# Optimization experiments

Hardware: AMD Instinct MI355X
Metric: run time of the kernel (lower is better)

Reference implementation:

```python
import jax, jax.numpy as jnp
import numpy as np

DIM = 512
HIDDEN = 1024
NUM_EXPERTS = 8
TOP_K = 2
BALANCE_LOSS_WEIGHT = 0.01


def setup_inputs() -> dict:
    key = jax.random.key(0)
    ks = jax.random.split(key, 6)
    B, S = 4, 8192
    x = jax.random.normal(ks[0], (B, S, DIM), dtype=jnp.float32)
    # Linear params (stored already transposed for x @ W convenience)
    scale_in = 1.0 / np.sqrt(DIM)
    scale_hid = 1.0 / np.sqrt(HIDDEN)
    gate_w = jax.random.uniform(ks[1], (DIM, NUM_EXPERTS), jnp.float32, -scale_in, scale_in)
    w1 = jax.random.uniform(ks[2], (NUM_EXPERTS, DIM, HIDDEN), jnp.float32, -scale_in, scale_in)
    b1 = jax.random.uniform(ks[3], (NUM_EXPERTS, HIDDEN), jnp.float32, -scale_in, scale_in)
    w2 = jax.random.uniform(ks[4], (NUM_EXPERTS, HIDDEN, DIM), jnp.float32, -scale_hid, scale_hid)
    b2 = jax.random.uniform(ks[5], (NUM_EXPERTS, DIM), jnp.float32, -scale_hid, scale_hid)
    return {"x": x, "gate_w": gate_w, "w1": w1, "b1": b1, "w2": w2, "b2": b2}


def reference(x, gate_w, w1, b1, w2, b2):
    B, S, D = x.shape
    T = B * S
    E = gate_w.shape[1]
    flat_x = x.reshape(T, D)

    # Gating (eval mode: no noise)
    gate_logits = flat_x @ gate_w                      # [T, E]
    gates = jax.nn.softmax(gate_logits, axis=-1)
    top_k_gates, top_k_indices = jax.lax.top_k(gates, TOP_K)
    top_k_gates = top_k_gates / jnp.sum(top_k_gates, axis=-1, keepdims=True)

    rows = jnp.arange(T)[:, None]
    # Per-token combine weight for each expert (0 if not selected)
    combine_w = jnp.zeros((T, E), flat_x.dtype).at[rows, top_k_indices].add(top_k_gates)
    # Load-balance loss (indices are discrete -> constant mask)
    expert_mask = jnp.zeros((T, E), flat_x.dtype).at[rows, top_k_indices].set(1.0)
    expert_usage = expert_mask.sum(0) / T
    balance_loss = jnp.mean((expert_usage - 1.0 / E) ** 2) * E * BALANCE_LOSS_WEIGHT

    # Expert MLPs; unselected tokens have combine weight 0 so contribute nothing,
    # matching the original masked gather/scatter math exactly.
    out = jnp.zeros_like(flat_x)
    for e in range(E):  # small fixed expert count
        h = jax.nn.gelu(flat_x @ w1[e] + b1[e], approximate=False)  # [T, HIDDEN]
        out = out + (h @ w2[e] + b2[e]) * combine_w[:, e:e + 1]
    return out.reshape(B, S, D), balance_loss
```

## Files before the change

### kernel.cpp

```cpp
#include <hip/hip_runtime.h>
#include <stdint.h>

#define T_TOK 32768
#define DDIM 512
#define HID 1024
#define NEXP 8

typedef _Float16 f16;
typedef _Float16 f16x8 __attribute__((ext_vector_type(8)));
typedef _Float16 f16x4 __attribute__((ext_vector_type(4)));
typedef float f32x4 __attribute__((ext_vector_type(4)));

__device__ __forceinline__ void gload_lds16(const void* g, void* l) {
  __builtin_amdgcn_global_load_lds(
      (__attribute__((address_space(1))) void*)g,
      (__attribute__((address_space(3))) void*)l, 16, 0, 0);
}

__global__ void k_cvt_x(const float* __restrict__ x, f16* __restrict__ xh) {
  int i = blockIdx.x * blockDim.x + threadIdx.x;
  float4 v = ((const float4*)x)[i];
  f16x4 o = {(f16)v.x, (f16)v.y, (f16)v.z, (f16)v.w};
  ((f16x4*)xh)[i] = o;
}

__global__ void k_transpose(const float* __restrict__ W, f16* __restrict__ Wt,
                            const int K, const int N) {
  __shared__ float tile[64][65];
  const int e = blockIdx.z;
  const float* Wb = W + (size_t)e * K * N;
  f16* Wtb = Wt + (size_t)e * K * N;
  const int k0 = blockIdx.x * 64, n0 = blockIdx.y * 64;
  const int tr = threadIdx.x >> 2;
  const int tc = (threadIdx.x & 3) * 16;
#pragma unroll
  for (int j = 0; j < 16; j += 4) {
    float4 v = *(const float4*)&Wb[(size_t)(k0 + tr) * N + n0 + tc + j];
    tile[tr][tc + j + 0] = v.x; tile[tr][tc + j + 1] = v.y;
    tile[tr][tc + j + 2] = v.z; tile[tr][tc + j + 3] = v.w;
  }
  __syncthreads();
  f16x8 t0, t1;
#pragma unroll
  for (int j = 0; j < 8; ++j) {
    t0[j] = (f16)tile[tc + j][tr];
    t1[j] = (f16)tile[tc + 8 + j][tr];
  }
  *(f16x8*)&Wtb[(size_t)(n0 + tr) * K + k0 + tc] = t0;
  *(f16x8*)&Wtb[(size_t)(n0 + tr) * K + k0 + tc + 8] = t1;
}

__global__ void k_gate(const float* __restrict__ x, const float* __restrict__ gw,
                       int* __restrict__ route_e, float* __restrict__ route_w,
                       int* __restrict__ cnt) {
  __shared__ int scnt[NEXP];
  const int tid = threadIdx.x, lane = tid & 63, wv = tid >> 6;
  if (tid < NEXP) scnt[tid] = 0;
  __syncthreads();

  float ga[4][8], gb[4][8];
#pragma unroll
  for (int j = 0; j < 4; ++j) {
    const int r0 = lane * 4 + j;
    const int r1 = 256 + lane * 4 + j;
    float4 q0 = *(const float4*)&gw[r0 * 8];
    float4 q1 = *(const float4*)&gw[r0 * 8 + 4];
    ga[j][0] = q0.x; ga[j][1] = q0.y; ga[j][2] = q0.z; ga[j][3] = q0.w;
    ga[j][4] = q1.x; ga[j][5] = q1.y; ga[j][6] = q1.z; ga[j][7] = q1.w;
    q0 = *(const float4*)&gw[r1 * 8];
    q1 = *(const float4*)&gw[r1 * 8 + 4];
    gb[j][0] = q0.x; gb[j][1] = q0.y; gb[j][2] = q0.z; gb[j][3] = q0.w;
    gb[j][4] = q1.x; gb[j][5] = q1.y; gb[j][6] = q1.z; gb[j][7] = q1.w;
  }

  const int tbase = blockIdx.x * 32 + wv * 8;
  for (int it = 0; it < 8; ++it) {
    const int t = tbase + it;
    const float4 A = *(const float4*)&x[(size_t)t * DDIM + lane * 4];
    const float4 B = *(const float4*)&x[(size_t)t * DDIM + 256 + lane * 4];
    float p[8];
#pragma unroll
    for (int e = 0; e < 8; ++e) {
      p[e] = A.x * ga[0][e] + A.y * ga[1][e] + A.z * ga[2][e] + A.w * ga[3][e] +
             B.x * gb[0][e] + B.y * gb[1][e] + B.z * gb[2][e] + B.w * gb[3][e];
    }
#pragma unroll
    for (int off = 32; off >= 1; off >>= 1) {
#pragma unroll
      for (int e = 0; e < 8; ++e) p[e] += __shfl_xor(p[e], off);
    }
    if (lane == 0) {
      int e1 = 0;
#pragma unroll
      for (int e = 1; e < 8; ++e) if (p[e] > p[e1]) e1 = e;
      int e2 = (e1 == 0) ? 1 : 0;
#pragma unroll
      for (int e = 0; e < 8; ++e) if (e != e1 && p[e] > p[e2]) e2 = e;
      const float wa = 1.0f / (1.0f + expf(p[e2] - p[e1]));
      route_e[t] = e1 | (e2 << 8);
      route_w[t] = wa;
      atomicAdd(&scnt[e1], 1);
      atomicAdd(&scnt[e2], 1);
    }
  }
  __syncthreads();
  if (tid < NEXP) atomicAdd(&cnt[tid], scnt[tid]);
}

__global__ void k_scan(const int* __restrict__ cnt, int* __restrict__ base,
                       int* __restrict__ cursor, float* __restrict__ out_loss) {
  if (threadIdx.x == 0) {
    int b = 0;
    float loss = 0.0f;
    for (int e = 0; e < NEXP; ++e) {
      base[e] = b;
      cursor[e] = b;
      b += cnt[e];
      float u = (float)cnt[e] / (float)T_TOK - 0.125f;
      loss += u * u;
    }
    *out_loss = loss * 0.01f;
  }
}

__global__ void k_scatter(const int* __restrict__ route_e, const float* __restrict__ route_w,
                          int* __restrict__ cursor, int* __restrict__ tok_slot,
                          float* __restrict__ wgt_slot) {
  const int t = blockIdx.x * blockDim.x + threadIdx.x;
  const int lane = threadIdx.x & 63;
  const int re = route_e[t];
  const float wa = route_w[t];
  const int e1 = re & 0xff, e2 = re >> 8;
#pragma unroll
  for (int e = 0; e < NEXP; ++e) {
    unsigned long long m = __ballot(e1 == e);
    if (m) {
      const int leader = __ffsll(m) - 1;
      int b0 = 0;
      if (lane == leader) b0 = atomicAdd(&cursor[e], __popcll(m));
      b0 = __shfl(b0, leader);
      if (e1 == e) {
        const int pos = b0 + __popcll(m & ((1ull << lane) - 1));
        tok_slot[pos] = t;
        wgt_slot[pos] = wa;
      }
    }
    m = __ballot(e2 == e);
    if (m) {
      const int leader = __ffsll(m) - 1;
      int b0 = 0;
      if (lane == leader) b0 = atomicAdd(&cursor[e], __popcll(m));
      b0 = __shfl(b0, leader);
      if (e2 == e) {
        const int pos = b0 + __popcll(m & ((1ull << lane) - 1));
        tok_slot[pos] = t;
        wgt_slot[pos] = 1.0f - wa;
      }
    }
  }
}


#define STAGE_G(k0_)                                                \
  do {                                                              \
    _Pragma("unroll") for (int i = 0; i < 4; ++i) {                 \
      gload_lds16(aSrc[i] + (k0_), &As0[(wv * 4 + i) * 512]);       \
      gload_lds16(bSrc[i] + (k0_), &Bs0[(wv * 4 + i) * 512]);       \
    }                                                               \
  } while (0)

#define COMPUTE(As_, Bs_)                                                         \
  do {                                                                            \
    _Pragma("unroll") for (int kb = 0; kb < 2; ++kb) {                            \
      f16x8 af[4], bf[4];                                                         \
      _Pragma("unroll") for (int mf = 0; mf < 4; ++mf) {                          \
        const int row = wm * 64 + mf * 16 + l15;                                  \
        af[mf] = *(const f16x8*)&(As_)[row * 64 + (((kb * 4 + g) ^ (row & 7)) * 8)]; \
      }                                                                           \
      _Pragma("unroll") for (int nf = 0; nf < 4; ++nf) {                          \
        const int row = wn * 64 + nf * 16 + l15;                                  \
        bf[nf] = *(const f16x8*)&(Bs_)[row * 64 + (((kb * 4 + g) ^ (row & 7)) * 8)]; \
      }                                                                           \
      _Pragma("unroll") for (int mf = 0; mf < 4; ++mf)                            \
        _Pragma("unroll") for (int nf = 0; nf < 4; ++nf)                          \
          acc[mf][nf] =                                                           \
              __builtin_amdgcn_mfma_f32_16x16x32_f16(af[mf], bf[nf], acc[mf][nf], 0, 0, 0); \
    }                                                                             \
  } while (0)

#define PIPE_LOOP(NT_)                                              \
  do {                                                              \
    for (int t = 0; t < (NT_); ++t) {                               \
      STAGE_G(t * 64);                                              \
      __syncthreads();             \
      COMPUTE(As0, Bs0);                                            \
      __syncthreads();                       \
    }                                                               \
  } while (0)

#define DECODE_SWZ(nN_)                                             \
  const int grp = 8 * (nN_);                                        \
  const int m_lin = (blockIdx.x / grp) * 8 + (blockIdx.x & 7);      \
  const int n0t = (blockIdx.x % grp) >> 3;                          \
  const int e = m_lin >> 6;                                         \
  const int mt = m_lin & 63;

__global__ __launch_bounds__(256, 4) void k_mlp1(
    const f16* __restrict__ xh, const f16* __restrict__ w1t,
    const float* __restrict__ b1, f16* __restrict__ h,
    const int* __restrict__ tok_slot, const int* __restrict__ base,
    const int* __restrict__ cnt, const int hc, const int c0, const int nN) {
  DECODE_SWZ(nN);
  const int ne = cnt[e];
  const int n0 = n0t * 128;
  const int sbase = base[e];
  const int shi = sbase + ne;

  __shared__ f16 As0[128 * 64];
  __shared__ f16 Bs0[128 * 64];

  const int tid = threadIdx.x;
  const int lane = tid & 63;
  const int wv = tid >> 6;
  const int wm = wv >> 1, wn = wv & 1;
  const int g = lane >> 4;
  const int l15 = lane & 15;

  for (int m0 = mt * 128; m0 < ne; m0 += 8192) {
    const int slot0 = sbase + m0;

    const f16* aSrc[4];
    const f16* bSrc[4];
#pragma unroll
    for (int i = 0; i < 4; ++i) {
      const int ch = wv * 4 + i;
      const int row = ch * 8 + (lane >> 3);
      const int sw = ((lane & 7) ^ (row & 7)) * 8;
      int slot = slot0 + row;
      slot = (slot <= shi - 1) ? slot : (shi - 1);
      const int tok = tok_slot[slot];
      aSrc[i] = xh + (size_t)tok * DDIM + sw;
      bSrc[i] = w1t + (size_t)(e * HID + c0 + n0 + row) * DDIM + sw;
    }

    f32x4 acc[4][4];
#pragma unroll
    for (int a = 0; a < 4; ++a)
#pragma unroll
      for (int b = 0; b < 4; ++b) { f32x4 z = {0.f, 0.f, 0.f, 0.f}; acc[a][b] = z; }

    PIPE_LOOP(DDIM / 64);

#pragma unroll
    for (int mf = 0; mf < 4; ++mf) {
#pragma unroll
      for (int r = 0; r < 4; ++r) {
        const int row = wm * 64 + mf * 16 + g * 4 + r;
        const int oslot = slot0 + row;
        if (oslot >= shi) continue;
#pragma unroll
        for (int nf = 0; nf < 4; ++nf) {
          const int col = wn * 64 + nf * 16 + l15;
          float v = acc[mf][nf][r] + b1[e * HID + c0 + n0 + col];
          v = 0.5f * v * (1.0f + erff(v * 0.70710678118654752f));
          h[(size_t)oslot * hc + n0 + col] = (f16)v;
        }
      }
    }
  }
}

__global__ __launch_bounds__(256, 4) void k_mlp2(
    const f16* __restrict__ h, const f16* __restrict__ w2t,
    const float* __restrict__ b2, float* __restrict__ out,
    const int* __restrict__ tok_slot, const float* __restrict__ wgt_slot,
    const int* __restrict__ base, const int* __restrict__ cnt,
    const int hc, const int c0) {
  DECODE_SWZ(4);
  const int ne = cnt[e];
  const int n0 = n0t * 128;
  const int sbase = base[e];
  const int shi = sbase + ne;

  __shared__ f16 As0[128 * 64];
  __shared__ f16 Bs0[128 * 64];

  const int tid = threadIdx.x;
  const int lane = tid & 63;
  const int wv = tid >> 6;
  const int wm = wv >> 1, wn = wv & 1;
  const int g = lane >> 4;
  const int l15 = lane & 15;

  for (int m0 = mt * 128; m0 < ne; m0 += 8192) {
    const int slot0 = sbase + m0;

    const f16* aSrc[4];
    const f16* bSrc[4];
#pragma unroll
    for (int i = 0; i < 4; ++i) {
      const int ch = wv * 4 + i;
      const int row = ch * 8 + (lane >> 3);
      const int sw = ((lane & 7) ^ (row & 7)) * 8;
      int slot = slot0 + row;
      slot = (slot <= shi - 1) ? slot : (shi - 1);
      aSrc[i] = h + (size_t)slot * hc + sw;
      bSrc[i] = w2t + (size_t)(e * DDIM + n0 + row) * HID + c0 + sw;
    }

    f32x4 acc[4][4];
#pragma unroll
    for (int a = 0; a < 4; ++a)
#pragma unroll
      for (int b = 0; b < 4; ++b) { f32x4 z = {0.f, 0.f, 0.f, 0.f}; acc[a][b] = z; }

    PIPE_LOOP(hc / 64);

#pragma unroll
    for (int mf = 0; mf < 4; ++mf) {
#pragma unroll
      for (int r = 0; r < 4; ++r) {
        const int row = wm * 64 + mf * 16 + g * 4 + r;
        const int oslot = slot0 + row;
        if (oslot >= shi) continue;
        const int tok = tok_slot[oslot];
        const float w = wgt_slot[oslot];
        float* orow = out + (size_t)tok * DDIM + n0;
#pragma unroll
        for (int nf = 0; nf < 4; ++nf) {
          const int col = wn * 64 + nf * 16 + l15;
          float v = acc[mf][nf][r];
          if (c0 == 0) v += b2[e * DDIM + n0 + col];
          unsafeAtomicAdd(orow + col, w * v);
        }
      }
    }
  }
}

extern "C" void kernel_launch(void* const* d_in, const int* in_sizes, int n_in,
                              void* d_out, int out_size, void* d_ws, size_t ws_size,
                              hipStream_t stream) {
  (void)in_sizes; (void)n_in;
  const float* x  = (const float*)d_in[0];
  const float* gw = (const float*)d_in[1];
  const float* w1 = (const float*)d_in[2];
  const float* b1 = (const float*)d_in[3];
  const float* w2 = (const float*)d_in[4];
  const float* b2 = (const float*)d_in[5];
  float* out = (float*)d_out;

  char* ws = (char*)d_ws;
  size_t off = 0;
  auto alloc = [&](size_t bytes) {
    char* p = ws + off;
    off += (bytes + 255) & ~(size_t)255;
    return p;
  };
  f16*   xh       = (f16*)  alloc((size_t)T_TOK * DDIM * 2);
  f16*   w1t      = (f16*)  alloc((size_t)NEXP * DDIM * HID * 2);
  f16*   w2t      = (f16*)  alloc((size_t)NEXP * DDIM * HID * 2);
  int*   route_e  = (int*)  alloc((size_t)T_TOK * 4);
  float* route_w  = (float*)alloc((size_t)T_TOK * 4);
  int*   tok_slot = (int*)  alloc((size_t)2 * T_TOK * 4);
  float* wgt_slot = (float*)alloc((size_t)2 * T_TOK * 4);
  int*   cnt      = (int*)  alloc(256);
  int*   base     = cnt + 8;
  int*   cursor   = cnt + 16;
  f16*   hbuf     = (f16*)(ws + off);
  const size_t havail = (ws_size > off) ? (ws_size - off) : 0;

  int ns = 4;
  const int cands[3] = {1, 2, 4};
  for (int i = 0; i < 3; ++i) {
    if ((size_t)2 * T_TOK * (HID / cands[i]) * 2 <= havail) { ns = cands[i]; break; }
  }
  const int hc = HID / ns;

  hipMemsetAsync(cnt, 0, 32, stream);
  hipMemsetAsync(d_out, 0, (size_t)out_size * sizeof(float), stream);

  k_cvt_x<<<dim3(T_TOK * DDIM / 4 / 256), 256, 0, stream>>>(x, xh);
  k_transpose<<<dim3(DDIM / 64, HID / 64, NEXP), 256, 0, stream>>>(w1, w1t, DDIM, HID);
  k_transpose<<<dim3(HID / 64, DDIM / 64, NEXP), 256, 0, stream>>>(w2, w2t, HID, DDIM);
  k_gate<<<dim3(T_TOK / 32), 256, 0, stream>>>(x, gw, route_e, route_w, cnt);
  k_scan<<<1, 64, 0, stream>>>(cnt, base, cursor, out + (size_t)T_TOK * DDIM);
  k_scatter<<<dim3(T_TOK / 256), 256, 0, stream>>>(route_e, route_w, cursor, tok_slot, wgt_slot);

  for (int c = 0; c < ns; ++c) {
    const int nN1 = hc / 128;
    k_mlp1<<<dim3(512 * nN1), 256, 0, stream>>>(
        xh, w1t, b1, hbuf, tok_slot, base, cnt, hc, c * hc, nN1);
    k_mlp2<<<dim3(512 * 4), 256, 0, stream>>>(
        hbuf, w2t, b2, out, tok_slot, wgt_slot, base, cnt, hc, c * hc);
  }
}
```

Baseline: 655.9 us.

## Widen MoE GEMM tiles to 128x256 with 512-thread blocks and unified LDS

Both expert GEMM kernels move from 128x128 output tiles with 4 waves to 128x256 tiles with 8 waves, staging A and B through one 384-row shared buffer. Each block now loads its gathered activation tile once for twice as many output columns, which cuts repeated A-side gathers and global traffic per flop. Block indexing changes from a swizzled grouping to expert-interleaved ordering, and a barrier is added at the end of each m-loop iteration. In exchange there are half as many blocks, more LDS per block, and lower occupancy.

```diff
diff --git a/kernel.cpp b/kernel.cpp
--- a/kernel.cpp
+++ b/kernel.cpp
@@ -163,23 +163,22 @@
 
 #define STAGE_G(k0_)                                                \
   do {                                                              \
-    _Pragma("unroll") for (int i = 0; i < 4; ++i) {                 \
-      gload_lds16(aSrc[i] + (k0_), &As0[(wv * 4 + i) * 512]);       \
-      gload_lds16(bSrc[i] + (k0_), &Bs0[(wv * 4 + i) * 512]);       \
+    _Pragma("unroll") for (int i = 0; i < 6; ++i) {                 \
+      gload_lds16(srcP[i] + (k0_), &S[(wv * 6 + i) * 512]);         \
     }                                                               \
   } while (0)
 
-#define COMPUTE(As_, Bs_)                                                         \
+#define COMPUTE()                                                                 \
   do {                                                                            \
     _Pragma("unroll") for (int kb = 0; kb < 2; ++kb) {                            \
       f16x8 af[4], bf[4];                                                         \
       _Pragma("unroll") for (int mf = 0; mf < 4; ++mf) {                          \
         const int row = wm * 64 + mf * 16 + l15;                                  \
-        af[mf] = *(const f16x8*)&(As_)[row * 64 + (((kb * 4 + g) ^ (row & 7)) * 8)]; \
+        af[mf] = *(const f16x8*)&S[row * 64 + (((kb * 4 + g) ^ (row & 7)) * 8)];  \
       }                                                                           \
       _Pragma("unroll") for (int nf = 0; nf < 4; ++nf) {                          \
-        const int row = wn * 64 + nf * 16 + l15;                                  \
-        bf[nf] = *(const f16x8*)&(Bs_)[row * 64 + (((kb * 4 + g) ^ (row & 7)) * 8)]; \
+        const int row = 128 + wn * 64 + nf * 16 + l15;                            \
+        bf[nf] = *(const f16x8*)&S[row * 64 + (((kb * 4 + g) ^ (row & 7)) * 8)];  \
       }                                                                           \
       _Pragma("unroll") for (int mf = 0; mf < 4; ++mf)                            \
         _Pragma("unroll") for (int nf = 0; nf < 4; ++nf)                          \
@@ -192,55 +191,56 @@
   do {                                                              \
     for (int t = 0; t < (NT_); ++t) {                               \
       STAGE_G(t * 64);                                              \
-      __syncthreads();             \
-      COMPUTE(As0, Bs0);                                            \
-      __syncthreads();                       \
+      __syncthreads();                                              \
+      COMPUTE();                                                    \
+      __syncthreads();                                              \
     }                                                               \
   } while (0)
 
-#define DECODE_SWZ(nN_)                                             \
-  const int grp = 8 * (nN_);                                        \
-  const int m_lin = (blockIdx.x / grp) * 8 + (blockIdx.x & 7);      \
-  const int n0t = (blockIdx.x % grp) >> 3;                          \
-  const int e = m_lin >> 6;                                         \
-  const int mt = m_lin & 63;
-
-__global__ __launch_bounds__(256, 4) void k_mlp1(
+__global__ __launch_bounds__(512, 2) void k_mlp1(
     const f16* __restrict__ xh, const f16* __restrict__ w1t,
     const float* __restrict__ b1, f16* __restrict__ h,
     const int* __restrict__ tok_slot, const int* __restrict__ base,
     const int* __restrict__ cnt, const int hc, const int c0, const int nN) {
-  DECODE_SWZ(nN);
+  const int e = blockIdx.x & 7;
+  const int q = blockIdx.x >> 3;
+  const int nt = q % nN;
+  const int mt = q / nN;
   const int ne = cnt[e];
-  const int n0 = n0t * 128;
+  const int n0 = nt * 256;
   const int sbase = base[e];
   const int shi = sbase + ne;
 
-  __shared__ f16 As0[128 * 64];
-  __shared__ f16 Bs0[128 * 64];
+  __shared__ f16 S[384 * 64];
 
   const int tid = threadIdx.x;
   const int lane = tid & 63;
   const int wv = tid >> 6;
-  const int wm = wv >> 1, wn = wv & 1;
+  const int wm = wv >> 2, wn = wv & 3;
   const int g = lane >> 4;
   const int l15 = lane & 15;
 
-  for (int m0 = mt * 128; m0 < ne; m0 += 8192) {
+  int sRow[6], sSw[6];
+#pragma unroll
+  for (int i = 0; i < 6; ++i) {
+    const int s = (wv * 6 + i) * 64 + lane;
+    sRow[i] = s >> 3;
+    sSw[i] = ((s & 7) ^ (sRow[i] & 7)) * 8;
+  }
+
+  for (int m0 = mt * 128; m0 < ne; m0 += 64 * 128) {
     const int slot0 = sbase + m0;
 
-    const f16* aSrc[4];
-    const f16* bSrc[4];
-#pragma unroll
-    for (int i = 0; i < 4; ++i) {
-      const int ch = wv * 4 + i;
-      const int row = ch * 8 + (lane >> 3);
-      const int sw = ((lane & 7) ^ (row & 7)) * 8;
-      int slot = slot0 + row;
-      slot = (slot <= shi - 1) ? slot : (shi - 1);
-      const int tok = tok_slot[slot];
-      aSrc[i] = xh + (size_t)tok * DDIM + sw;
-      bSrc[i] = w1t + (size_t)(e * HID + c0 + n0 + row) * DDIM + sw;
+    const f16* srcP[6];
+#pragma unroll
+    for (int i = 0; i < 6; ++i) {
+      if (sRow[i] < 128) {
+        int slot = slot0 + sRow[i];
+        slot = (slot <= shi - 1) ? slot : (shi - 1);
+        srcP[i] = xh + (size_t)tok_slot[slot] * DDIM + sSw[i];
+      } else {
+        srcP[i] = w1t + (size_t)(e * HID + c0 + n0 + sRow[i] - 128) * DDIM + sSw[i];
+      }
     }
 
     f32x4 acc[4][4];
@@ -267,45 +267,55 @@
         }
       }
     }
-  }
-}
-
-__global__ __launch_bounds__(256, 4) void k_mlp2(
+    __syncthreads();
+  }
+}
+
+__global__ __launch_bounds__(512, 2) void k_mlp2(
     const f16* __restrict__ h, const f16* __restrict__ w2t,
     const float* __restrict__ b2, float* __restrict__ out,
     const int* __restrict__ tok_slot, const float* __restrict__ wgt_slot,
     const int* __restrict__ base, const int* __restrict__ cnt,
     const int hc, const int c0) {
-  DECODE_SWZ(4);
+  const int e = blockIdx.x & 7;
+  const int q = blockIdx.x >> 3;
+  const int nt = q & 1;
+  const int mt = q >> 1;
   const int ne = cnt[e];
-  const int n0 = n0t * 128;
+  const int n0 = nt * 256;
   const int sbase = base[e];
   const int shi = sbase + ne;
 
-  __shared__ f16 As0[128 * 64];
-  __shared__ f16 Bs0[128 * 64];
+  __shared__ f16 S[384 * 64];
 
   const int tid = threadIdx.x;
   const int lane = tid & 63;
   const int wv = tid >> 6;
-  const int wm = wv >> 1, wn = wv & 1;
+  const int wm = wv >> 2, wn = wv & 3;
   const int g = lane >> 4;
   const int l15 = lane & 15;
 
-  for (int m0 = mt * 128; m0 < ne; m0 += 8192) {
+  int sRow[6], sSw[6];
+#pragma unroll
+  for (int i = 0; i < 6; ++i) {
+    const int s = (wv * 6 + i) * 64 + lane;
+    sRow[i] = s >> 3;
+    sSw[i] = ((s & 7) ^ (sRow[i] & 7)) * 8;
+  }
+
+  for (int m0 = mt * 128; m0 < ne; m0 += 64 * 128) {
     const int slot0 = sbase + m0;
 
-    const f16* aSrc[4];
-    const f16* bSrc[4];
-#pragma unroll
-    for (int i = 0; i < 4; ++i) {
-      const int ch = wv * 4 + i;
-      const int row = ch * 8 + (lane >> 3);
-      const int sw = ((lane & 7) ^ (row & 7)) * 8;
-      int slot = slot0 + row;
-      slot = (slot <= shi - 1) ? slot : (shi - 1);
-      aSrc[i] = h + (size_t)slot * hc + sw;
-      bSrc[i] = w2t + (size_t)(e * DDIM + n0 + row) * HID + c0 + sw;
+    const f16* srcP[6];
+#pragma unroll
+    for (int i = 0; i < 6; ++i) {
+      if (sRow[i] < 128) {
+        int slot = slot0 + sRow[i];
+        slot = (slot <= shi - 1) ? slot : (shi - 1);
+        srcP[i] = h + (size_t)slot * hc + sSw[i];
+      } else {
+        srcP[i] = w2t + (size_t)(e * DDIM + n0 + sRow[i] - 128) * HID + c0 + sSw[i];
+      }
     }
 
     f32x4 acc[4][4];
@@ -335,6 +345,7 @@
         }
       }
     }
+    __syncthreads();
   }
 }
 
@@ -388,10 +399,10 @@
   k_scatter<<<dim3(T_TOK / 256), 256, 0, stream>>>(route_e, route_w, cursor, tok_slot, wgt_slot);
 
   for (int c = 0; c < ns; ++c) {
-    const int nN1 = hc / 128;
-    k_mlp1<<<dim3(512 * nN1), 256, 0, stream>>>(
+    const int nN1 = hc / 256;
+    k_mlp1<<<dim3(8 * 64 * nN1), 512, 0, stream>>>(
         xh, w1t, b1, hbuf, tok_slot, base, cnt, hc, c * hc, nN1);
-    k_mlp2<<<dim3(512 * 4), 256, 0, stream>>>(
+    k_mlp2<<<dim3(8 * 64 * 2), 512, 0, stream>>>(
         hbuf, w2t, b2, out, tok_slot, wgt_slot, base, cnt, hc, c * hc);
   }
 }
```

Result: slower. 677.0 us (+3.2%).
